# Kernel tuning notes

Measured on AMD Instinct MI355X. Metric: run time of the kernel, lower is better.

Reference implementation:

```python
import jax, jax.numpy as jnp
import numpy as np

N, IN_C, OUT_C, H = 100000, 256, 64, 8
K_CURV = 1.0      # manifold curvature k (Lorentz: t = sqrt(||s||^2 + k))
POWER_K = 2.0     # power_k of fp feature map


def fp(x, p):
    # norm(x) / (norm(x**p) + eps) * x**p, norms over last dim
    eps = 1e-12
    xp = x ** p
    norm_x = jnp.linalg.norm(x, axis=-1, keepdims=True)
    norm_xp = jnp.linalg.norm(xp, axis=-1, keepdims=True)
    return norm_x / (norm_xp + eps) * xp


def setup_inputs() -> dict:
    key = jax.random.key(0)
    ks = jax.random.split(key, 8)
    s = 1.0 / np.sqrt(IN_C)
    sm = 1.0 / np.sqrt(OUT_C)
    return {
        "query_input": jax.random.normal(ks[0], (N, IN_C), jnp.float32),
        # per-head HypLinear weights (stacked over heads)
        "Wq": jax.random.uniform(ks[1], (H, IN_C, OUT_C), jnp.float32, -s, s),
        "bq": jnp.zeros((H, OUT_C), jnp.float32),
        "Wk": jax.random.uniform(ks[2], (H, IN_C, OUT_C), jnp.float32, -s, s),
        "bk": jnp.zeros((H, OUT_C), jnp.float32),
        "Wv": jax.random.uniform(ks[3], (H, IN_C, OUT_C), jnp.float32, -s, s),
        "bv": jnp.zeros((H, OUT_C), jnp.float32),
        "norm_scale": jnp.ones((), jnp.float32),
        # v_map_mlp: Linear(out_channels, out_channels)
        "Wm": jax.random.uniform(ks[4], (OUT_C, OUT_C), jnp.float32, -sm, sm),
        "bm": jnp.zeros((OUT_C,), jnp.float32),
    }


def reference(query_input, Wq, bq, Wk, bk, Wv, bv, norm_scale, Wm, bm):
    # HypLinear per head: space part = x @ W + b; the time part
    # sqrt(||space||^2 + k) is dropped by [..., 1:] in linear_focus_attention,
    # so only the space components are computed.  shapes: [N, H, OUT_C]
    qs = jnp.einsum('nd,hdo->nho', query_input, Wq) + bq
    ks_ = jnp.einsum('nd,hdo->nho', query_input, Wk) + bk
    v = jnp.einsum('nd,hdo->nho', query_input, Wv) + bv

    denom_s = jnp.abs(norm_scale) + 1e-6
    phi_q = fp((jax.nn.relu(qs) + 1e-6) / denom_s, POWER_K)
    phi_k = fp((jax.nn.relu(ks_) + 1e-6) / denom_s, POWER_K)

    # linear attention: O(N * H * m * d)
    kT_v = jnp.einsum('nhm,nhd->hmd', phi_k, v)          # [H, m, d]
    numerator = jnp.einsum('nhm,hmd->nhd', phi_q, kT_v)  # [N, H, d]
    sum_k = phi_k.sum(axis=0)                            # [H, m]
    denominator = jnp.einsum('nhd,hd->nh', phi_q, sum_k)[..., None]
    attn = numerator / (denominator + 1e-6)

    # residual v-map MLP
    attn = attn + (jnp.einsum('nhd,de->nhe', v, Wm) + bm)

    # trans_heads_concat=False -> mean over heads
    out = attn.mean(axis=1)                              # [N, OUT_C]

    # lift back to Lorentz: prepend time component
    t = jnp.sqrt((out ** 2).sum(axis=-1, keepdims=True) + K_CURV)
    return jnp.concatenate([t, out], axis=-1)            # [N, OUT_C+1]
```

## Files before the change

### kernel.cpp

```cpp
#include <hip/hip_runtime.h>
#include <hip/hip_bf16.h>

#define NROWS 100000
#define NH 8
#define RPC 1568
#define NSUB 49
#define NCH1 64

typedef short s16x8 __attribute__((ext_vector_type(8)));
typedef float f32x4 __attribute__((ext_vector_type(4)));
typedef unsigned short u16;

__device__ __forceinline__ u16 f2bf(float f) {
  union { float f; unsigned u; } x; x.f = f;
  unsigned r = (x.u + 0x7FFFu + ((x.u >> 16) & 1u)) >> 16;
  return (u16)r;
}
__device__ __forceinline__ float bf2f(u16 b) {
  union { unsigned u; float f; } x; x.u = ((unsigned)b) << 16;
  return x.f;
}

__global__ __launch_bounds__(256) void k0_pack(
    const float* __restrict__ Wq, const float* __restrict__ Wk,
    const float* __restrict__ Wv, u16* __restrict__ Wp)
{
  int t = blockIdx.x * 256 + threadIdx.x;
  int lane = t & 63;
  int rest = t >> 6;
  int s = rest % 48;
  int hc = rest / 48;
  int c2 = hc & 1, h = hc >> 1;
  int ml = lane & 15, sgk = lane >> 4;
  const float* W; int col, ks;
  if (s < 32) { int tl = s >> 3; ks = s & 7; W = c2 ? Wk : Wq; col = tl * 16 + ml; }
  else        { int tv = (s >> 3) - 4; ks = s & 7; W = Wv; col = c2 * 32 + tv * 16 + ml; }
  int k0 = ks * 32 + sgk * 8;
  u16 o[8];
#pragma unroll
  for (int j = 0; j < 8; j++)
    o[j] = f2bf(W[((size_t)h * 256 + k0 + j) * 64 + col]);
  ushort4* dst = (ushort4*)(Wp + (size_t)t * 8);
  dst[0] = make_ushort4(o[0], o[1], o[2], o[3]);
  dst[1] = make_ushort4(o[4], o[5], o[6], o[7]);
}

__global__ __launch_bounds__(256, 2) void k1_gemm_phi(
    const float* __restrict__ x, const u16* __restrict__ Wp,
    const float* __restrict__ bq, const float* __restrict__ bk,
    const float* __restrict__ bv, const float* __restrict__ nsc,
    u16* __restrict__ phi_q, u16* __restrict__ vout, float* __restrict__ P)
{
  __shared__ u16 xs[32 * 256];
  __shared__ u16 vws[32 * 64 * 8];
  __shared__ u16 stq[4 * 16 * 72];
  __shared__ u16 stv[32 * 72];
  __shared__ u16 tks[64 * 40];
  __shared__ u16 tvs[64 * 40];
  __shared__ float biasl[192];

  const int tid = threadIdx.x;
  const int wv = tid >> 6, lane = tid & 63;
  const int c2 = wv & 1, rg = wv >> 1;
  const int m = lane & 15, sg = lane >> 4;
  const int rc = blockIdx.x & 63, h = blockIdx.x >> 6;
  const int n0 = rc * RPC;

  if (tid < 192) {
    const float* bp = tid < 64 ? bq : (tid < 128 ? bk : bv);
    biasl[tid] = bp[h * 64 + (tid & 63)];
  }

  const u16* wb = Wp + (size_t)(h * 2 + c2) * (48 * 64 * 8);
  s16x8 wq[4][8];
#pragma unroll
  for (int t = 0; t < 4; t++)
#pragma unroll
    for (int ks = 0; ks < 8; ks++)
      wq[t][ks] = *(const s16x8*)(wb + ((t * 8 + ks) * 64 + lane) * 8);

#pragma unroll
  for (int i2 = 0; i2 < 8; i2++) {
    int u = tid + i2 * 256;
    int tl = u >> 9, ks = (u >> 6) & 7, ln = u & 63;
    const u16* src = Wp + ((size_t)(h * 2 + (tl >> 1)) * 48 + 32 + (tl & 1) * 8 + ks) * (64 * 8)
                     + (size_t)ln * 8;
    *(s16x8*)(vws + (size_t)u * 8) = *(const s16x8*)src;
  }

#pragma unroll
  for (int i = 0; i < 4; i++) {
    int cu = tid + i * 256;
    int row = cu >> 5, c = cu & 31;
    int n = n0 + row; if (n >= NROWS) n = NROWS - 1;
    const float* src = x + (size_t)n * 256 + c * 8;
    float4 f0 = *(const float4*)src;
    float4 f1 = *(const float4*)(src + 4);
    s16x8 pk;
    pk[0] = (short)f2bf(f0.x); pk[1] = (short)f2bf(f0.y);
    pk[2] = (short)f2bf(f0.z); pk[3] = (short)f2bf(f0.w);
    pk[4] = (short)f2bf(f1.x); pk[5] = (short)f2bf(f1.y);
    pk[6] = (short)f2bf(f1.z); pk[7] = (short)f2bf(f1.w);
    *(s16x8*)(xs + row * 256 + ((c ^ (row & 7)) * 8)) = pk;
  }
  __syncthreads();

  const float inv_denom = 1.0f / (fabsf(nsc[0]) + 1e-6f);
  u16* const xbase = xs + (rg * 16 + m) * 256;
  const int sw = m & 7;

  f32x4 kacc[4];
#pragma unroll
  for (int t = 0; t < 4; t++) kacc[t] = (f32x4){0.f, 0.f, 0.f, 0.f};
  f32x4 ksum = (f32x4){0.f, 0.f, 0.f, 0.f};
  s16x8 onesf;
#pragma unroll
  for (int j = 0; j < 8; j++) onesf[j] = (m == 0) ? (short)0x3F80 : (short)0;

  for (int s = 0; s < NSUB; s++) {
    float4 xl[8];
    if (s + 1 < NSUB) {
      int nb = n0 + (s + 1) * 32;
#pragma unroll
      for (int i = 0; i < 4; i++) {
        int cu = tid + i * 256;
        int row = cu >> 5, c = cu & 31;
        int n = nb + row; if (n >= NROWS) n = NROWS - 1;
        const float* src = x + (size_t)n * 256 + c * 8;
        xl[i * 2]     = *(const float4*)src;
        xl[i * 2 + 1] = *(const float4*)(src + 4);
      }
    }

    f32x4 aq[4], av[2];
#pragma unroll
    for (int t = 0; t < 4; t++) aq[t] = (f32x4){0.f, 0.f, 0.f, 0.f};
    av[0] = (f32x4){0.f, 0.f, 0.f, 0.f};
    av[1] = (f32x4){0.f, 0.f, 0.f, 0.f};
#pragma unroll
    for (int ks = 0; ks < 8; ks++) {
      s16x8 bf = *(const s16x8*)(xbase + (((ks * 4 + sg) ^ sw) * 8));
#pragma unroll
      for (int t = 0; t < 4; t++)
        aq[t] = __builtin_amdgcn_mfma_f32_16x16x32_bf16(wq[t][ks], bf, aq[t], 0, 0, 0);
      s16x8 vw0 = *(const s16x8*)(vws + (((c2 * 2 + 0) * 8 + ks) * 64 + lane) * 8);
      s16x8 vw1 = *(const s16x8*)(vws + (((c2 * 2 + 1) * 8 + ks) * 64 + lane) * 8);
      av[0] = __builtin_amdgcn_mfma_f32_16x16x32_bf16(vw0, bf, av[0], 0, 0, 0);
      av[1] = __builtin_amdgcn_mfma_f32_16x16x32_bf16(vw1, bf, av[1], 0, 0, 0);
    }

    f32x4 bqk[4], bvv[2];
#pragma unroll
    for (int t = 0; t < 4; t++) bqk[t] = *(const f32x4*)&biasl[c2 * 64 + t * 16 + sg * 4];
#pragma unroll
    for (int tv = 0; tv < 2; tv++) bvv[tv] = *(const f32x4*)&biasl[128 + c2 * 32 + tv * 16 + sg * 4];

    float vq[4][4];
    float s2 = 0.f, s4 = 0.f;
#pragma unroll
    for (int t = 0; t < 4; t++)
#pragma unroll
      for (int r = 0; r < 4; r++) {
        float y = (fmaxf(aq[t][r] + bqk[t][r], 0.f) + 1e-6f) * inv_denom;
        float y2 = y * y;
        vq[t][r] = y2;
        s2 += y2; s4 += y2 * y2;
      }
    s2 += __shfl_xor(s2, 16); s2 += __shfl_xor(s2, 32);
    s4 += __shfl_xor(s4, 16); s4 += __shfl_xor(s4, 32);
    float sc = sqrtf(s2) / (sqrtf(s4) + 1e-12f);

    {
      int rowl = rg * 16 + m;
      if (!c2) {
        u16* sq = stq + wv * 1152 + m * 72;
#pragma unroll
        for (int t = 0; t < 4; t++)
          *(ushort4*)(sq + ((t + m) & 3) * 16 + sg * 4) =
            make_ushort4(f2bf(vq[t][0] * sc), f2bf(vq[t][1] * sc),
                         f2bf(vq[t][2] * sc), f2bf(vq[t][3] * sc));
      } else {
#pragma unroll
        for (int t = 0; t < 4; t++)
#pragma unroll
          for (int r = 0; r < 4; r++)
            tks[(t * 16 + sg * 4 + r) * 40 + rowl] = f2bf(vq[t][r] * sc);
      }
      u16* sv = stv + rowl * 72;
#pragma unroll
      for (int tv = 0; tv < 2; tv++) {
        int tc = c2 * 2 + tv;
        f32x4 a = av[tv], b = bvv[tv];
        u16 e0 = f2bf(a[0] + b[0]), e1 = f2bf(a[1] + b[1]);
        u16 e2 = f2bf(a[2] + b[2]), e3 = f2bf(a[3] + b[3]);
        *(ushort4*)(sv + ((tc + rowl) & 3) * 16 + sg * 4) = make_ushort4(e0, e1, e2, e3);
        int chb = (tc * 16 + sg * 4) * 40 + rowl;
        tvs[chb]       = e0;
        tvs[chb + 40]  = e1;
        tvs[chb + 80]  = e2;
        tvs[chb + 120] = e3;
      }
    }
    if (!c2) {
      int r_ = lane >> 2, tc = lane & 3;
      const u16* a = stq + wv * 1152 + r_ * 72 + ((tc + r_) & 3) * 16;
      s16x8 p0 = *(const s16x8*)a;
      s16x8 p1 = *(const s16x8*)(a + 8);
      int n = n0 + s * 32 + rg * 16 + r_;
      if (n < NROWS) {
        u16* dst = phi_q + ((size_t)h * NROWS + n) * 64 + tc * 16;
        *(s16x8*)dst = p0;
        *(s16x8*)(dst + 8) = p1;
      }
    }
    __syncthreads();

    {
      int row = wv * 8 + (lane >> 3);
      int hc8 = lane & 7, tc = hc8 >> 1, half = hc8 & 1;
      const u16* a = stv + row * 72 + ((tc + row) & 3) * 16 + half * 8;
      s16x8 pv = *(const s16x8*)a;
      int n = n0 + s * 32 + row;
      if (n < NROWS)
        *(s16x8*)(vout + ((size_t)h * NROWS + n) * 64 + tc * 16 + half * 8) = pv;
    }

    if (n0 + s * 32 < NROWS) {
      s16x8 af = *(const s16x8*)(tks + (wv * 16 + m) * 40 + sg * 8);
#pragma unroll
      for (int dcb = 0; dcb < 4; dcb++) {
        s16x8 bfv = *(const s16x8*)(tvs + (dcb * 16 + m) * 40 + sg * 8);
        kacc[dcb] = __builtin_amdgcn_mfma_f32_16x16x32_bf16(af, bfv, kacc[dcb], 0, 0, 0);
      }
      ksum = __builtin_amdgcn_mfma_f32_16x16x32_bf16(af, onesf, ksum, 0, 0, 0);
    }

    if (s + 1 < NSUB) {
#pragma unroll
      for (int i = 0; i < 4; i++) {
        int cu = tid + i * 256;
        int row = cu >> 5, c = cu & 31;
        float4 f0 = xl[i * 2], f1 = xl[i * 2 + 1];
        s16x8 pk;
        pk[0] = (short)f2bf(f0.x); pk[1] = (short)f2bf(f0.y);
        pk[2] = (short)f2bf(f0.z); pk[3] = (short)f2bf(f0.w);
        pk[4] = (short)f2bf(f1.x); pk[5] = (short)f2bf(f1.y);
        pk[6] = (short)f2bf(f1.z); pk[7] = (short)f2bf(f1.w);
        *(s16x8*)(xs + row * 256 + ((c ^ (row & 7)) * 8)) = pk;
      }
    }
    __syncthreads();
  }

  {
    float* pb = P + (size_t)(rc * NH + h) * (65 * 64);
    int mm = wv * 16 + sg * 4;
#pragma unroll
    for (int dcb = 0; dcb < 4; dcb++)
#pragma unroll
      for (int r = 0; r < 4; r++)
        pb[(dcb * 16 + m) * 64 + mm + r] = kacc[dcb][r];
    if (m == 0)
#pragma unroll
      for (int r = 0; r < 4; r++)
        pb[64 * 64 + mm + r] = ksum[r];
  }
}

__global__ __launch_bounds__(256) void k25_pack(
    const float* __restrict__ P, const float* __restrict__ Wm,
    u16* __restrict__ kTvT, u16* __restrict__ WmP)
{
  int idx = blockIdx.x * 256 + threadIdx.x;
  if (idx < NH * 65 * 64) {
    float s = 0.f;
    for (int rcc = 0; rcc < NCH1; rcc++)
      s += P[(size_t)rcc * (NH * 65 * 64) + idx];
    kTvT[idx] = f2bf(s);
  } else if (idx < NH * 65 * 64 + 64 * 64) {
    int j = idx - NH * 65 * 64;
    WmP[j] = f2bf(Wm[(j & 63) * 64 + (j >> 6)]);
  }
}

__global__ __launch_bounds__(256) void k3_out(
    const u16* __restrict__ phi_q, const u16* __restrict__ vin,
    const u16* __restrict__ kTvT, const u16* __restrict__ WmP,
    const float* __restrict__ bm, float* __restrict__ out)
{
  const int tid = threadIdx.x;
  const int wv = tid >> 6, lane = tid & 63;
  const int m = lane & 15, sg = lane >> 4;
  const int n0 = blockIdx.x * 64;
  const int rw = wv * 16;
  const int n = n0 + rw + m;

  float bmv[4];
#pragma unroll
  for (int t = 0; t < 4; t++) bmv[t] = bm[t * 16 + m];

  s16x8 vbf[2];
#pragma unroll
  for (int ks = 0; ks < 2; ks++) {
    float a[8];
#pragma unroll
    for (int j = 0; j < 8; j++) a[j] = 0.f;
#pragma unroll
    for (int h = 0; h < NH; h++) {
      s16x8 v8 = *(const s16x8*)(vin + (size_t)h * (NROWS * 64) + (size_t)n * 64
                                 + ks * 32 + sg * 8);
#pragma unroll
      for (int j = 0; j < 8; j++) a[j] += bf2f((u16)v8[j]);
    }
#pragma unroll
    for (int j = 0; j < 8; j++) vbf[ks][j] = (short)f2bf(a[j] * 0.125f);
  }

  f32x4 zero4 = {0.f, 0.f, 0.f, 0.f};
  s16x8 zero8 = {0, 0, 0, 0, 0, 0, 0, 0};
  f32x4 osum[4];
#pragma unroll
  for (int t = 0; t < 4; t++) osum[t] = zero4;

  for (int h = 0; h < NH; h++) {
    const u16* pqb = phi_q + (size_t)h * (NROWS * 64) + (size_t)n * 64;
    const u16* kb = kTvT + (size_t)h * (65 * 64);
    f32x4 accn[4];
#pragma unroll
    for (int t = 0; t < 4; t++) accn[t] = zero4;
    f32x4 accd = zero4;
#pragma unroll
    for (int ks = 0; ks < 2; ks++) {
      s16x8 aq = *(const s16x8*)(pqb + ks * 32 + sg * 8);
#pragma unroll
      for (int t = 0; t < 4; t++) {
        s16x8 bfv = *(const s16x8*)(kb + (size_t)(t * 16 + m) * 64 + ks * 32 + sg * 8);
        accn[t] = __builtin_amdgcn_mfma_f32_16x16x32_bf16(aq, bfv, accn[t], 0, 0, 0);
      }
      s16x8 bd = zero8;
      if (m == 0)
        bd = *(const s16x8*)(kb + (size_t)64 * 64 + ks * 32 + sg * 8);
      accd = __builtin_amdgcn_mfma_f32_16x16x32_bf16(aq, bd, accd, 0, 0, 0);
    }
#pragma unroll
    for (int r = 0; r < 4; r++) {
      float den = __shfl(accd[r], lane & 48);
      float rinv = 1.0f / (den + 1e-6f);
#pragma unroll
      for (int t = 0; t < 4; t++) osum[t][r] += accn[t][r] * rinv;
    }
  }

  f32x4 accr[4];
#pragma unroll
  for (int t = 0; t < 4; t++) accr[t] = zero4;
#pragma unroll
  for (int ks = 0; ks < 2; ks++)
#pragma unroll
    for (int t = 0; t < 4; t++) {
      s16x8 bw = *(const s16x8*)(WmP + (size_t)(t * 16 + m) * 64 + ks * 32 + sg * 8);
      accr[t] = __builtin_amdgcn_mfma_f32_16x16x32_bf16(vbf[ks], bw, accr[t], 0, 0, 0);
    }

#pragma unroll
  for (int r = 0; r < 4; r++) {
    int nn = n0 + rw + sg * 4 + r;
    float v4[4];
    float ssq = 0.f;
#pragma unroll
    for (int t = 0; t < 4; t++) {
      float o = osum[t][r] * 0.125f + accr[t][r] + bmv[t];
      v4[t] = o;
      ssq += o * o;
    }
    ssq += __shfl_xor(ssq, 1);
    ssq += __shfl_xor(ssq, 2);
    ssq += __shfl_xor(ssq, 4);
    ssq += __shfl_xor(ssq, 8);
    if (nn < NROWS) {
      if (m == 0) out[(size_t)nn * 65] = sqrtf(ssq + 1.0f);
#pragma unroll
      for (int t = 0; t < 4; t++)
        out[(size_t)nn * 65 + 1 + t * 16 + m] = v4[t];
    }
  }
}

extern "C" void kernel_launch(void* const* d_in, const int* in_sizes, int n_in,
                              void* d_out, int out_size, void* d_ws, size_t ws_size,
                              hipStream_t stream) {
  const float* x   = (const float*)d_in[0];
  const float* Wq  = (const float*)d_in[1];
  const float* bq  = (const float*)d_in[2];
  const float* Wk  = (const float*)d_in[3];
  const float* bk  = (const float*)d_in[4];
  const float* Wv  = (const float*)d_in[5];
  const float* bv  = (const float*)d_in[6];
  const float* nsc = (const float*)d_in[7];
  const float* Wm  = (const float*)d_in[8];
  const float* bm  = (const float*)d_in[9];
  float* out = (float*)d_out;

  char* ws = (char*)d_ws;
  const size_t PHI_BYTES = (size_t)NROWS * NH * 64 * 2;
  u16* phi_q = (u16*)(ws);
  u16* vv    = (u16*)(ws + PHI_BYTES);
  u16* Wp    = (u16*)(ws + 2 * PHI_BYTES);
  char* p    = ws + 2 * PHI_BYTES + 786432;
  float* P   = (float*)(p);
  u16* kTvT  = (u16*)(p + 8519680);
  u16* WmP   = (u16*)(p + 8519680 + 66560);

  k0_pack<<<192, 256, 0, stream>>>(Wq, Wk, Wv, Wp);
  k1_gemm_phi<<<512, 256, 0, stream>>>(x, Wp, bq, bk, bv, nsc, phi_q, vv, P);
  k25_pack<<<(NH * 65 * 64 + 64 * 64 + 255) / 256, 256, 0, stream>>>(P, Wm, kTvT, WmP);
  k3_out<<<(NROWS + 63) / 64, 256, 0, stream>>>(phi_q, vv, kTvT, WmP, bm, out);
}
```

Baseline: 490.2 us.

## Double-buffer K/V tiles with transpose LDS reads and defer kTv MFMA

Replaces the scattered scalar LDS stores of phi_k and v (transposed layout) with vectorized ushort4 stores into a row-major double-buffered layout, and reads them back with ds_read_b64_tr_b16 transpose loads. The kTv accumulation for sub-tile s-1 is moved to the start of iteration s, so it overlaps with the next projection GEMM instead of sitting after a barrier. The stq staging buffer is shrunk by indexing it per row group. This adds inline asm with a full lgkmcnt wait and a sched barrier, which may constrain scheduling.

```diff
diff --git a/kernel.cpp b/kernel.cpp
--- a/kernel.cpp
+++ b/kernel.cpp
@@ -8,6 +8,7 @@
 #define NCH1 64
 
 typedef short s16x8 __attribute__((ext_vector_type(8)));
+typedef short s16x4 __attribute__((ext_vector_type(4)));
 typedef float f32x4 __attribute__((ext_vector_type(4)));
 typedef unsigned short u16;
 
@@ -53,10 +54,10 @@
 {
   __shared__ u16 xs[32 * 256];
   __shared__ u16 vws[32 * 64 * 8];
-  __shared__ u16 stq[4 * 16 * 72];
+  __shared__ u16 stq[2 * 16 * 72];
   __shared__ u16 stv[32 * 72];
-  __shared__ u16 tks[64 * 40];
-  __shared__ u16 tvs[64 * 40];
+  __shared__ u16 tks[2 * 2048];
+  __shared__ u16 tvs[2 * 2048];
   __shared__ float biasl[192];
 
   const int tid = threadIdx.x;
@@ -65,6 +66,9 @@
   const int m = lane & 15, sg = lane >> 4;
   const int rc = blockIdx.x & 63, h = blockIdx.x >> 6;
   const int n0 = rc * RPC;
+
+  const unsigned tks_lds = (unsigned)(size_t)&tks[0];
+  const unsigned tvs_lds = (unsigned)(size_t)&tvs[0];
 
   if (tid < 192) {
     const float* bp = tid < 64 ? bq : (tid < 128 ? bk : bv);
@@ -117,6 +121,35 @@
 #pragma unroll
   for (int j = 0; j < 8; j++) onesf[j] = (m == 0) ? (short)0x3F80 : (short)0;
 
+#define KTV_ACC(pb)                                                           \
+  {                                                                           \
+    const unsigned ak  = tks_lds + (unsigned)((pb) * 4096 + sg * 1024 + wv * 128 + m * 2); \
+    const unsigned avr = tvs_lds + (unsigned)((pb) * 4096 + sg * 1024 + m * 2); \
+    s16x4 k0_, k1_, b0l, b0h, b1l, b1h, b2l, b2h, b3l, b3h;                   \
+    asm volatile("ds_read_b64_tr_b16 %0, %1 offset:0"   : "=v"(k0_) : "v"(ak));  \
+    asm volatile("ds_read_b64_tr_b16 %0, %1 offset:512" : "=v"(k1_) : "v"(ak));  \
+    asm volatile("ds_read_b64_tr_b16 %0, %1 offset:0"   : "=v"(b0l) : "v"(avr)); \
+    asm volatile("ds_read_b64_tr_b16 %0, %1 offset:512" : "=v"(b0h) : "v"(avr)); \
+    asm volatile("ds_read_b64_tr_b16 %0, %1 offset:128" : "=v"(b1l) : "v"(avr)); \
+    asm volatile("ds_read_b64_tr_b16 %0, %1 offset:640" : "=v"(b1h) : "v"(avr)); \
+    asm volatile("ds_read_b64_tr_b16 %0, %1 offset:256" : "=v"(b2l) : "v"(avr)); \
+    asm volatile("ds_read_b64_tr_b16 %0, %1 offset:768" : "=v"(b2h) : "v"(avr)); \
+    asm volatile("ds_read_b64_tr_b16 %0, %1 offset:384" : "=v"(b3l) : "v"(avr)); \
+    asm volatile("ds_read_b64_tr_b16 %0, %1 offset:896" : "=v"(b3h) : "v"(avr)); \
+    asm volatile("s_waitcnt lgkmcnt(0)" ::: "memory");                        \
+    __builtin_amdgcn_sched_barrier(0);                                        \
+    s16x8 af  = __builtin_shufflevector(k0_, k1_, 0, 1, 2, 3, 4, 5, 6, 7);    \
+    s16x8 bv0 = __builtin_shufflevector(b0l, b0h, 0, 1, 2, 3, 4, 5, 6, 7);    \
+    s16x8 bv1 = __builtin_shufflevector(b1l, b1h, 0, 1, 2, 3, 4, 5, 6, 7);    \
+    s16x8 bv2 = __builtin_shufflevector(b2l, b2h, 0, 1, 2, 3, 4, 5, 6, 7);    \
+    s16x8 bv3 = __builtin_shufflevector(b3l, b3h, 0, 1, 2, 3, 4, 5, 6, 7);    \
+    kacc[0] = __builtin_amdgcn_mfma_f32_16x16x32_bf16(af, bv0, kacc[0], 0, 0, 0); \
+    kacc[1] = __builtin_amdgcn_mfma_f32_16x16x32_bf16(af, bv1, kacc[1], 0, 0, 0); \
+    kacc[2] = __builtin_amdgcn_mfma_f32_16x16x32_bf16(af, bv2, kacc[2], 0, 0, 0); \
+    kacc[3] = __builtin_amdgcn_mfma_f32_16x16x32_bf16(af, bv3, kacc[3], 0, 0, 0); \
+    ksum    = __builtin_amdgcn_mfma_f32_16x16x32_bf16(af, onesf, ksum, 0, 0, 0);  \
+  }
+
   for (int s = 0; s < NSUB; s++) {
     float4 xl[8];
     if (s + 1 < NSUB) {
@@ -132,6 +165,8 @@
       }
     }
 
+    if (s > 0 && n0 + (s - 1) * 32 < NROWS) KTV_ACC((s - 1) & 1);
+
     f32x4 aq[4], av[2];
 #pragma unroll
     for (int t = 0; t < 4; t++) aq[t] = (f32x4){0.f, 0.f, 0.f, 0.f};
@@ -172,8 +207,9 @@
 
     {
       int rowl = rg * 16 + m;
+      int sb = (s & 1) * 2048 + (rowl >> 2) * 256 + (rowl & 3) * 16 + sg * 4;
       if (!c2) {
-        u16* sq = stq + wv * 1152 + m * 72;
+        u16* sq = stq + rg * 1152 + m * 72;
 #pragma unroll
         for (int t = 0; t < 4; t++)
           *(ushort4*)(sq + ((t + m) & 3) * 16 + sg * 4) =
@@ -182,9 +218,9 @@
       } else {
 #pragma unroll
         for (int t = 0; t < 4; t++)
-#pragma unroll
-          for (int r = 0; r < 4; r++)
-            tks[(t * 16 + sg * 4 + r) * 40 + rowl] = f2bf(vq[t][r] * sc);
+          *(ushort4*)(tks + sb + t * 64) =
+            make_ushort4(f2bf(vq[t][0] * sc), f2bf(vq[t][1] * sc),
+                         f2bf(vq[t][2] * sc), f2bf(vq[t][3] * sc));
       }
       u16* sv = stv + rowl * 72;
 #pragma unroll
@@ -194,16 +230,12 @@
         u16 e0 = f2bf(a[0] + b[0]), e1 = f2bf(a[1] + b[1]);
         u16 e2 = f2bf(a[2] + b[2]), e3 = f2bf(a[3] + b[3]);
         *(ushort4*)(sv + ((tc + rowl) & 3) * 16 + sg * 4) = make_ushort4(e0, e1, e2, e3);
-        int chb = (tc * 16 + sg * 4) * 40 + rowl;
-        tvs[chb]       = e0;
-        tvs[chb + 40]  = e1;
-        tvs[chb + 80]  = e2;
-        tvs[chb + 120] = e3;
+        *(ushort4*)(tvs + sb + tc * 64) = make_ushort4(e0, e1, e2, e3);
       }
     }
     if (!c2) {
       int r_ = lane >> 2, tc = lane & 3;
-      const u16* a = stq + wv * 1152 + r_ * 72 + ((tc + r_) & 3) * 16;
+      const u16* a = stq + rg * 1152 + r_ * 72 + ((tc + r_) & 3) * 16;
       s16x8 p0 = *(const s16x8*)a;
       s16x8 p1 = *(const s16x8*)(a + 8);
       int n = n0 + s * 32 + rg * 16 + r_;
@@ -223,16 +255,6 @@
       int n = n0 + s * 32 + row;
       if (n < NROWS)
         *(s16x8*)(vout + ((size_t)h * NROWS + n) * 64 + tc * 16 + half * 8) = pv;
-    }
-
-    if (n0 + s * 32 < NROWS) {
-      s16x8 af = *(const s16x8*)(tks + (wv * 16 + m) * 40 + sg * 8);
-#pragma unroll
-      for (int dcb = 0; dcb < 4; dcb++) {
-        s16x8 bfv = *(const s16x8*)(tvs + (dcb * 16 + m) * 40 + sg * 8);
-        kacc[dcb] = __builtin_amdgcn_mfma_f32_16x16x32_bf16(af, bfv, kacc[dcb], 0, 0, 0);
-      }
-      ksum = __builtin_amdgcn_mfma_f32_16x16x32_bf16(af, onesf, ksum, 0, 0, 0);
     }
 
     if (s + 1 < NSUB) {
@@ -251,6 +273,8 @@
     }
     __syncthreads();
   }
+
+  if (n0 + (NSUB - 1) * 32 < NROWS) KTV_ACC((NSUB - 1) & 1);
 
   {
     float* pb = P + (size_t)(rc * NH + h) * (65 * 64);
```

Result: slower. 550.5 us (+12.3%).
